# Performance work log

Measured on AMD Instinct MI355X. Metric: run time of the kernel, lower is better.

The kernel has to match this reference:

```python
import jax, jax.numpy as jnp
import numpy as np

N_NODES = 100000
N_EDGES = 1600000
D_IN = 256
D_HID = 128
N_CLASSES = 64
NEG_SLOPE = 0.2


def setup_inputs() -> dict:
    key = jax.random.key(0)
    ks = jax.random.split(key, 8)
    node_features = jax.random.normal(ks[0], (N_NODES, D_IN), dtype=jnp.float32)
    W = jax.random.normal(ks[1], (D_IN, D_HID), dtype=jnp.float32) * (1.0 / np.sqrt(D_IN))
    attn_l = jax.random.normal(ks[2], (D_HID,), dtype=jnp.float32) * (1.0 / np.sqrt(D_HID))
    attn_r = jax.random.normal(ks[3], (D_HID,), dtype=jnp.float32) * (1.0 / np.sqrt(D_HID))
    fc_W = jax.random.normal(ks[4], (D_HID, N_CLASSES), dtype=jnp.float32) * (1.0 / np.sqrt(D_HID))
    fc_b = jnp.zeros((N_CLASSES,), dtype=jnp.float32)
    src = jax.random.randint(ks[5], (N_EDGES,), 0, N_NODES, dtype=jnp.int32)
    dst = jax.random.randint(ks[6], (N_EDGES,), 0, N_NODES, dtype=jnp.int32)
    return dict(node_features=node_features, W=W, attn_l=attn_l, attn_r=attn_r,
                fc_W=fc_W, fc_b=fc_b, src=src, dst=dst)


def reference(node_features, W, attn_l, attn_r, fc_W, fc_b, src, dst):
    N = node_features.shape[0]
    # GATConv (single head): linear projection
    feat = node_features @ W                       # [N, H]
    el = feat @ attn_l                             # [N]
    er = feat @ attn_r                             # [N]
    e = jax.nn.leaky_relu(el[src] + er[dst], NEG_SLOPE)  # [E]
    # segment softmax over incoming edges of each destination node
    m = jax.ops.segment_max(e, dst, num_segments=N)      # [N]
    ex = jnp.exp(e - m[dst])                              # [E]
    denom = jax.ops.segment_sum(ex, dst, num_segments=N)  # [N]
    a = ex / denom[dst]                                   # [E]
    # attention-weighted neighbor aggregation (scatter-add)
    msg = a[:, None] * feat[src]                           # [E, H]
    h = jax.ops.segment_sum(msg, dst, num_segments=N)     # [N, H]
    # num_heads=1 -> h.mean(1) over heads is identity; final Linear
    return h @ fc_W + fc_b                                 # [N, C]
```

## Files before the change

### kernel.cpp

```cpp
#include <hip/hip_runtime.h>
#include <math.h>

#define NN 100000
#define NE 1600000
#define DIN 256
#define DHID 128
#define NCLS 64
#define NEG_SLOPE 0.2f

#define NBUCK 196
#define ECAP 10240
#define CHUNK 4096
#define NCHB ((NE + CHUNK - 1) / CHUNK)
#define PREPB 16

#define NGRP 16384
#define G1 ((NN + 127) / 128)

typedef __bf16 bf16_t;
typedef bf16_t bf16x8 __attribute__((ext_vector_type(8)));
typedef float f32x4 __attribute__((ext_vector_type(4)));
typedef ushort ushort8v __attribute__((ext_vector_type(8)));

__device__ __forceinline__ ushort f2bf(float f) {
    union { float f; unsigned u; } c; c.f = f;
    unsigned u = c.u;
    unsigned r = (u + 0x7FFFu + ((u >> 16) & 1u)) >> 16;
    return (ushort)r;
}
__device__ __forceinline__ float bf2f(ushort b) {
    return __uint_as_float(((unsigned)b) << 16);
}

__global__ __launch_bounds__(256) void k_prep(const float* __restrict__ W,
                                              const float* __restrict__ fcW,
                                              ushort* __restrict__ Wt,
                                              ushort* __restrict__ fcWt,
                                              int* __restrict__ gcur) {
    int t = blockIdx.x * 256 + threadIdx.x;
    if (blockIdx.x == 0) gcur[threadIdx.x] = 0;
    for (int i = t; i < DHID * DIN; i += PREPB * 256) {
        int n = i >> 8, k = i & 255;
        Wt[i] = f2bf(W[k * DHID + n]);
    }
    for (int i = t; i < NCLS * DHID; i += PREPB * 256) {
        int n = i >> 7, k = i & 127;
        fcWt[i] = f2bf(fcW[k * NCLS + n]);
    }
}

union SmemB {
    struct {
        int hist[NBUCK];
        int scn[256];
        int loff[NBUCK];
        int cur[NBUCK];
        int gb[NBUCK];
        unsigned ord[CHUNK];
        ushort obk[CHUNK];
    } b;
    struct {
        ushort Xs[2][8192];
        ushort Wl[2][8192];
        float Al[DHID];
        float Ar[DHID];
    } g;
};

__global__ __launch_bounds__(256, 2) void fused_bin_gemm1(
        const int* __restrict__ src, const int* __restrict__ dst,
        int* __restrict__ gcur, unsigned* __restrict__ ebuf,
        const float* __restrict__ X, const ushort* __restrict__ Wt,
        const float* __restrict__ attn_l, const float* __restrict__ attn_r,
        ushort* __restrict__ featb, float* __restrict__ el, float* __restrict__ er) {
    __shared__ SmemB sm;
    const int t = threadIdx.x;

    if (blockIdx.x < NCHB) {
        const int base = blockIdx.x * CHUNK;
        int cnt = NE - base; if (cnt > CHUNK) cnt = CHUNK;

        for (int i = t; i < NBUCK; i += 256) sm.b.hist[i] = 0;
        __syncthreads();

        unsigned vals[16];
        int bks[16];
#pragma unroll
        for (int i = 0; i < 16; i++) {
            int idx = base + i * 256 + t;
            if (idx < NE) {
                int d = dst[idx], s = src[idx];
                int bb = d >> 9;
                bks[i] = bb;
                vals[i] = ((unsigned)(d & 511) << 17) | (unsigned)s;
                atomicAdd(&sm.b.hist[bb], 1);
            } else bks[i] = -1;
        }
        __syncthreads();

        int hv = (t < NBUCK) ? sm.b.hist[t] : 0;
        sm.b.scn[t] = hv;
        __syncthreads();
        for (int d = 1; d < 256; d <<= 1) {
            int a = (t >= d) ? sm.b.scn[t - d] : 0;
            __syncthreads();
            sm.b.scn[t] += a;
            __syncthreads();
        }
        if (t < NBUCK) { sm.b.loff[t] = sm.b.scn[t] - hv; sm.b.cur[t] = sm.b.scn[t] - hv; }
        __syncthreads();

#pragma unroll
        for (int i = 0; i < 16; i++) {
            if (bks[i] >= 0) {
                int slot = atomicAdd(&sm.b.cur[bks[i]], 1);
                sm.b.ord[slot] = vals[i];
                sm.b.obk[slot] = (ushort)bks[i];
            }
        }
        if (t < NBUCK && hv > 0) sm.b.gb[t] = t * ECAP + atomicAdd(&gcur[t], hv);
        __syncthreads();

        for (int s = t; s < cnt; s += 256) {
            int bb = sm.b.obk[s];
            ebuf[sm.b.gb[bb] + (s - sm.b.loff[bb])] = sm.b.ord[s];
        }
        return;
    }

    const int row0 = (blockIdx.x - NCHB) * 128;
    if (t < 128) { sm.g.Al[t] = attn_l[t]; sm.g.Ar[t] = attn_r[t]; }

    int srow[4], ske[4];
#pragma unroll
    for (int i = 0; i < 4; i++) {
        int o = i * 4096 + t * 16;
        int row = o >> 7;
        int bl = (o & 127) ^ ((row & 7) << 4);
        srow[i] = row;
        ske[i] = bl >> 1;
    }

    float4 xr[4][2];
    uint4  wr[4];

#pragma unroll
    for (int i = 0; i < 4; i++) {
        int grow = row0 + srow[i];
        if (grow < NN) {
            const float4* p = (const float4*)(X + (size_t)grow * DIN + ske[i]);
            xr[i][0] = p[0]; xr[i][1] = p[1];
        } else {
            xr[i][0] = make_float4(0.f, 0.f, 0.f, 0.f);
            xr[i][1] = make_float4(0.f, 0.f, 0.f, 0.f);
        }
        wr[i] = *(const uint4*)(Wt + (size_t)srow[i] * DIN + ske[i]);
    }
#pragma unroll
    for (int i = 0; i < 4; i++) {
        int o = i * 4096 + t * 16;
        ushort8v b;
        b[0] = f2bf(xr[i][0].x); b[1] = f2bf(xr[i][0].y);
        b[2] = f2bf(xr[i][0].z); b[3] = f2bf(xr[i][0].w);
        b[4] = f2bf(xr[i][1].x); b[5] = f2bf(xr[i][1].y);
        b[6] = f2bf(xr[i][1].z); b[7] = f2bf(xr[i][1].w);
        *(ushort8v*)((char*)&sm.g.Xs[0][0] + o) = b;
        *(uint4*)((char*)&sm.g.Wl[0][0] + o) = wr[i];
    }
    __syncthreads();

    const int w = t >> 6, lane = t & 63;
    const int rbase = w * 32;
    const int lcol = lane & 15;
    const int kgrp = (lane >> 4) * 16;

    f32x4 acc[2][8];
#pragma unroll
    for (int r = 0; r < 2; r++)
#pragma unroll
        for (int c = 0; c < 8; c++) acc[r][c] = (f32x4){0.f, 0.f, 0.f, 0.f};

    for (int c = 0; c < 4; c++) {
        const int buf = c & 1;
        if (c < 3) {
            int k0g = (c + 1) * 64;
#pragma unroll
            for (int i = 0; i < 4; i++) {
                int grow = row0 + srow[i];
                if (grow < NN) {
                    const float4* p = (const float4*)(X + (size_t)grow * DIN + k0g + ske[i]);
                    xr[i][0] = p[0]; xr[i][1] = p[1];
                } else {
                    xr[i][0] = make_float4(0.f, 0.f, 0.f, 0.f);
                    xr[i][1] = make_float4(0.f, 0.f, 0.f, 0.f);
                }
                wr[i] = *(const uint4*)(Wt + (size_t)srow[i] * DIN + k0g + ske[i]);
            }
        }
        const char* xb = (const char*)&sm.g.Xs[buf][0];
        const char* wb = (const char*)&sm.g.Wl[buf][0];
#pragma unroll
        for (int k0 = 0; k0 < 2; k0++) {
            int kb = k0 * 64 + kgrp;
            bf16x8 a[2], b[8];
#pragma unroll
            for (int r = 0; r < 2; r++) {
                int row = rbase + r * 16 + lcol;
                a[r] = *(const bf16x8*)(xb + row * 128 + (kb ^ ((row & 7) << 4)));
            }
#pragma unroll
            for (int cc = 0; cc < 8; cc++) {
                int n = cc * 16 + lcol;
                b[cc] = *(const bf16x8*)(wb + n * 128 + (kb ^ ((n & 7) << 4)));
            }
#pragma unroll
            for (int r = 0; r < 2; r++)
#pragma unroll
                for (int cc = 0; cc < 8; cc++)
                    acc[r][cc] = __builtin_amdgcn_mfma_f32_16x16x32_bf16(a[r], b[cc], acc[r][cc], 0, 0, 0);
        }
        if (c < 3) {
#pragma unroll
            for (int i = 0; i < 4; i++) {
                int o = i * 4096 + t * 16;
                ushort8v b;
                b[0] = f2bf(xr[i][0].x); b[1] = f2bf(xr[i][0].y);
                b[2] = f2bf(xr[i][0].z); b[3] = f2bf(xr[i][0].w);
                b[4] = f2bf(xr[i][1].x); b[5] = f2bf(xr[i][1].y);
                b[6] = f2bf(xr[i][1].z); b[7] = f2bf(xr[i][1].w);
                *(ushort8v*)((char*)&sm.g.Xs[buf ^ 1][0] + o) = b;
                *(uint4*)((char*)&sm.g.Wl[buf ^ 1][0] + o) = wr[i];
            }
        }
        __syncthreads();
    }

    ushort* Os = (ushort*)sm.g.Xs;
#pragma unroll
    for (int r = 0; r < 2; r++)
#pragma unroll
        for (int cc = 0; cc < 8; cc++)
#pragma unroll
            for (int i = 0; i < 4; i++) {
                int rloc = rbase + r * 16 + (lane >> 4) * 4 + i;
                int col = cc * 16 + lcol;
                Os[rloc * 128 + col] = f2bf(acc[r][cc][i]);
            }
    __syncthreads();

    {
        int row = t >> 1, half = t & 1;
        int grow = row0 + row;
        const ushort* orow = Os + row * 128 + half * 64;
        const float* alp = sm.g.Al + half * 64;
        const float* arp = sm.g.Ar + half * 64;
        float pl = 0.f, pr = 0.f;
        int rot = row & 7;
#pragma unroll
        for (int qq = 0; qq < 8; qq++) {
            int q = (qq + rot) & 7;
            ushort8v f8 = *(const ushort8v*)(orow + q * 8);
#pragma unroll
            for (int e = 0; e < 8; e++) {
                float fe = bf2f(f8[e]);
                pl += fe * alp[q * 8 + e];
                pr += fe * arp[q * 8 + e];
            }
        }
        pl += __shfl_down(pl, 1);
        pr += __shfl_down(pr, 1);
        if (!half && grow < NN) { el[grow] = pl; er[grow] = pr; }
    }

#pragma unroll
    for (int i = 0; i < 8; i++) {
        int u = i * 256 + t;
        int row = u >> 4;
        int grow = row0 + row;
        if (grow < NN)
            *(uint4*)(featb + (size_t)grow * 128 + (u & 15) * 8) =
                *(uint4*)((char*)Os + u * 16);
    }
}

union SmemC {
    struct {
        int sdeg[512];
        int pr[256];
        int lofs[512];
        int scnt[512];
    } c;
    int sh[256];
};

__global__ __launch_bounds__(256) void fused_csr(const unsigned* __restrict__ ebuf,
                                                 const int* __restrict__ gcur,
                                                 int* __restrict__ off_g,
                                                 int* __restrict__ deg_g,
                                                 int* __restrict__ ssrc,
                                                 int* __restrict__ bpre) {
    __shared__ SmemC sm;
    const int t = threadIdx.x;

    if (blockIdx.x == NBUCK) {
        int v = (t < NBUCK) ? gcur[t] : 0;
        sm.sh[t] = v;
        __syncthreads();
        for (int d = 1; d < 256; d <<= 1) {
            int a = (t >= d) ? sm.sh[t - d] : 0;
            __syncthreads();
            sm.sh[t] += a;
            __syncthreads();
        }
        if (t < NBUCK) bpre[t] = sm.sh[t] - v;
        if (t == NBUCK - 1) bpre[NBUCK] = sm.sh[t];
        return;
    }

    const int b = blockIdx.x;
    const int node0 = b << 9;
    const int ebase = b * ECAP;
    const int ecnt = gcur[b];

    sm.c.sdeg[t] = 0; sm.c.sdeg[t + 256] = 0;
    __syncthreads();
    for (int s = t; s < ecnt; s += 256)
        atomicAdd(&sm.c.sdeg[ebuf[ebase + s] >> 17], 1);
    __syncthreads();

    int d0 = sm.c.sdeg[2 * t], d1 = sm.c.sdeg[2 * t + 1];
    sm.c.pr[t] = d0 + d1;
    __syncthreads();
    for (int d = 1; d < 256; d <<= 1) {
        int a = (t >= d) ? sm.c.pr[t - d] : 0;
        __syncthreads();
        sm.c.pr[t] += a;
        __syncthreads();
    }
    int ex = sm.c.pr[t] - d0 - d1;
    sm.c.lofs[2 * t] = ex;
    sm.c.lofs[2 * t + 1] = ex + d0;
    sm.c.scnt[2 * t] = 0; sm.c.scnt[2 * t + 1] = 0;
    int n0 = node0 + 2 * t, n1 = n0 + 1;
    if (n0 < NN) { off_g[n0] = ebase + ex;      deg_g[n0] = d0; }
    if (n1 < NN) { off_g[n1] = ebase + ex + d0; deg_g[n1] = d1; }
    __syncthreads();

    for (int s = t; s < ecnt; s += 256) {
        unsigned v = ebuf[ebase + s];
        int dl = v >> 17;
        int c = atomicAdd(&sm.c.scnt[dl], 1);
        ssrc[ebase + sm.c.lofs[dl] + c] = (int)(v & 0x1FFFFu);
    }
}

__global__ __launch_bounds__(256) void k_split(const int* __restrict__ off,
                                               const int* __restrict__ bpre,
                                               int* __restrict__ nsplit) {
    int g = blockIdx.x * 256 + threadIdx.x;
    if (g > NGRP) return;
    if (g == NGRP) { nsplit[NGRP] = NN; return; }
    long total = bpre[NBUCK];
    long target = (long)g * total / NGRP;
    int lo = 0, hi = NN;
    while (lo < hi) {
        int mid = (lo + hi) >> 1;
        int b = mid >> 9;
        long real = (long)off[mid] - (long)b * ECAP + bpre[b];
        if (real < target) lo = mid + 1; else hi = mid;
    }
    nsplit[g] = lo;
}

__global__ __launch_bounds__(256) void aggregate(const int* __restrict__ off,
                                                 const int* __restrict__ deg,
                                                 const int* __restrict__ ssrc,
                                                 const float* __restrict__ el,
                                                 const float* __restrict__ er,
                                                 const ushort* __restrict__ featb,
                                                 ushort* __restrict__ hb,
                                                 const int* __restrict__ nsplit) {
    const int gid = blockIdx.x * 16 + (threadIdx.x >> 4);
    const int lc = threadIdx.x & 15;
    int n = nsplit[gid];
    const int nend = nsplit[gid + 1];
    const ushort* fb = featb + lc * 8;

    for (; n < nend; ++n) {
        const int e0 = off[n];
        const int dg = deg[n];
        const float erd = er[n];
        float acc[8];
#pragma unroll
        for (int q = 0; q < 8; q++) acc[q] = 0.f;
        float wsum = 0.f;

        int j = 0;
        for (; j + 4 <= dg; j += 4) {
            int s0 = ssrc[e0 + j + 0];
            int s1 = ssrc[e0 + j + 1];
            int s2 = ssrc[e0 + j + 2];
            int s3 = ssrc[e0 + j + 3];
            ushort8v f0 = *(const ushort8v*)(fb + (size_t)s0 * DHID);
            ushort8v f1 = *(const ushort8v*)(fb + (size_t)s1 * DHID);
            ushort8v f2 = *(const ushort8v*)(fb + (size_t)s2 * DHID);
            ushort8v f3 = *(const ushort8v*)(fb + (size_t)s3 * DHID);
            float x0 = el[s0] + erd, x1 = el[s1] + erd;
            float x2 = el[s2] + erd, x3 = el[s3] + erd;
            x0 = x0 > 0.f ? x0 : NEG_SLOPE * x0;
            x1 = x1 > 0.f ? x1 : NEG_SLOPE * x1;
            x2 = x2 > 0.f ? x2 : NEG_SLOPE * x2;
            x3 = x3 > 0.f ? x3 : NEG_SLOPE * x3;
            float w0 = __expf(x0), w1 = __expf(x1);
            float w2 = __expf(x2), w3 = __expf(x3);
            wsum += (w0 + w1) + (w2 + w3);
#pragma unroll
            for (int q = 0; q < 8; q++)
                acc[q] += (w0 * bf2f(f0[q]) + w1 * bf2f(f1[q])) +
                          (w2 * bf2f(f2[q]) + w3 * bf2f(f3[q]));
        }
        for (; j < dg; ++j) {
            int s0 = ssrc[e0 + j];
            ushort8v f0 = *(const ushort8v*)(fb + (size_t)s0 * DHID);
            float x0 = el[s0] + erd;
            x0 = x0 > 0.f ? x0 : NEG_SLOPE * x0;
            float w0 = __expf(x0);
            wsum += w0;
#pragma unroll
            for (int q = 0; q < 8; q++) acc[q] += w0 * bf2f(f0[q]);
        }

        float inv = (dg > 0) ? 1.0f / wsum : 0.f;
        ushort8v o8;
#pragma unroll
        for (int q = 0; q < 8; q++) o8[q] = f2bf(acc[q] * inv);
        *(ushort8v*)(hb + (size_t)n * DHID + lc * 8) = o8;
    }
}

__global__ __launch_bounds__(256, 3) void gemm2(const ushort* __restrict__ hb,
                                                const ushort* __restrict__ fcWt,
                                                const float* __restrict__ fcb,
                                                float* __restrict__ out) {
    __shared__ ushort Hs[128 * 128];
    __shared__ ushort Fs[64 * 128];
    const int t = threadIdx.x;
    const int row0 = blockIdx.x * 128;

    {
#pragma unroll
        for (int i = 0; i < 8; i++) {
            int u = i * 256 + t;
            int row = u >> 4;
            int grow = row0 + row;
            uint4 v = make_uint4(0, 0, 0, 0);
            if (grow < NN) v = *(const uint4*)(hb + (size_t)grow * 128 + (u & 15) * 8);
            int byte_off = row * 256 + (((u & 15) * 16) ^ ((row & 7) << 4));
            *(uint4*)((char*)Hs + byte_off) = v;
        }
#pragma unroll
        for (int i = 0; i < 4; i++) {
            int u = i * 256 + t;
            int n = u >> 4;
            int byte_off = n * 256 + (((u & 15) * 16) ^ ((n & 7) << 4));
            *(uint4*)((char*)Fs + byte_off) = ((const uint4*)fcWt)[u];
        }
    }

    const int w = t >> 6, lane = t & 63;
    const int rbase = w * 32;
    const int lcol = lane & 15;
    const int kgrp = (lane >> 4) * 16;

    f32x4 acc[2][4];
#pragma unroll
    for (int c = 0; c < 4; c++) {
        float bias = fcb[c * 16 + lcol];
#pragma unroll
        for (int r = 0; r < 2; r++)
#pragma unroll
            for (int i = 0; i < 4; i++) acc[r][c][i] = bias;
    }
    __syncthreads();

#pragma unroll
    for (int k0 = 0; k0 < 4; k0++) {
        int kbyte = k0 * 64 + kgrp;
        bf16x8 a[2], b[4];
#pragma unroll
        for (int r = 0; r < 2; r++) {
            int row = rbase + r * 16 + lcol;
            a[r] = *(bf16x8*)((char*)Hs + row * 256 + (kbyte ^ ((row & 7) << 4)));
        }
#pragma unroll
        for (int c = 0; c < 4; c++) {
            int n = c * 16 + lcol;
            b[c] = *(bf16x8*)((char*)Fs + n * 256 + (kbyte ^ ((n & 7) << 4)));
        }
#pragma unroll
        for (int r = 0; r < 2; r++)
#pragma unroll
            for (int c = 0; c < 4; c++)
                acc[r][c] = __builtin_amdgcn_mfma_f32_16x16x32_bf16(a[r], b[c], acc[r][c], 0, 0, 0);
    }

#pragma unroll
    for (int r = 0; r < 2; r++)
#pragma unroll
        for (int i = 0; i < 4; i++) {
            int row = rbase + r * 16 + (lane >> 4) * 4 + i;
            int grow = row0 + row;
            if (grow < NN) {
                float* op = out + (size_t)grow * 64 + lcol;
#pragma unroll
                for (int c = 0; c < 4; c++) op[c * 16] = acc[r][c][i];
            }
        }
}

extern "C" void kernel_launch(void* const* d_in, const int* in_sizes, int n_in,
                              void* d_out, int out_size, void* d_ws, size_t ws_size,
                              hipStream_t stream) {
    const float* X      = (const float*)d_in[0];
    const float* W      = (const float*)d_in[1];
    const float* attn_l = (const float*)d_in[2];
    const float* attn_r = (const float*)d_in[3];
    const float* fcW    = (const float*)d_in[4];
    const float* fcb    = (const float*)d_in[5];
    const int*   src    = (const int*)d_in[6];
    const int*   dst    = (const int*)d_in[7];
    float* out = (float*)d_out;

    char* ws = (char*)d_ws;
    ushort* featb = (ushort*)ws;            ws += (size_t)NN * DHID * 2;
    ushort* hb    = (ushort*)ws;            ws += (size_t)NN * DHID * 2;
    ushort* Wt    = (ushort*)ws;            ws += (size_t)DHID * DIN * 2;
    ushort* fcWt  = (ushort*)ws;            ws += (size_t)NCLS * DHID * 2;
    float* el     = (float*)ws;             ws += (size_t)NN * 4;
    float* er     = (float*)ws;             ws += (size_t)NN * 4;
    int*   deg    = (int*)ws;               ws += (size_t)NN * 4;
    int*   off    = (int*)ws;               ws += (size_t)NN * 4;
    int*   ssrc   = (int*)ws;               ws += (size_t)NBUCK * ECAP * 4;
    unsigned* ebuf = (unsigned*)ws;         ws += (size_t)NBUCK * ECAP * 4;
    int*   gcur   = (int*)ws;               ws += (size_t)256 * 4;
    int*   bpre   = (int*)ws;               ws += (size_t)256 * 4;
    int*   nsplit = (int*)ws;               ws += (size_t)(NGRP + 1) * 4;

    k_prep<<<PREPB, 256, 0, stream>>>(W, fcW, Wt, fcWt, gcur);
    fused_bin_gemm1<<<NCHB + G1, 256, 0, stream>>>(src, dst, gcur, ebuf,
                                                   X, Wt, attn_l, attn_r, featb, el, er);
    fused_csr<<<NBUCK + 1, 256, 0, stream>>>(ebuf, gcur, off, deg, ssrc, bpre);
    k_split<<<(NGRP + 256) / 256, 256, 0, stream>>>(off, bpre, nsplit);
    aggregate<<<NGRP / 16, 256, 0, stream>>>(off, deg, ssrc, el, er, featb, hb, nsplit);
    gemm2<<<(NN + 127) / 128, 256, 0, stream>>>(hb, fcWt, fcb, out);
}
```

Before: 160.4 us.

## Fuse bucket prefix and split search into CSR kernel; deepen GEMM prefetch

```diff
diff --git a/kernel.cpp b/kernel.cpp
--- a/kernel.cpp
+++ b/kernel.cpp
@@ -67,6 +67,61 @@
     } g;
 };
 
+#define ISSUE(XA, WA, KC) do { \
+    int k0g_ = (KC) * 64; \
+    _Pragma("unroll") \
+    for (int i_ = 0; i_ < 4; i_++) { \
+        int grow_ = row0 + srow[i_]; \
+        if (grow_ < NN) { \
+            const float4* p_ = (const float4*)(X + (size_t)grow_ * DIN + k0g_ + ske[i_]); \
+            XA[i_][0] = p_[0]; XA[i_][1] = p_[1]; \
+        } else { \
+            XA[i_][0] = make_float4(0.f,0.f,0.f,0.f); \
+            XA[i_][1] = make_float4(0.f,0.f,0.f,0.f); \
+        } \
+        WA[i_] = *(const uint4*)(Wt + (size_t)srow[i_] * DIN + k0g_ + ske[i_]); \
+    } \
+} while (0)
+
+#define COMMIT(XA, WA, BUF) do { \
+    _Pragma("unroll") \
+    for (int i_ = 0; i_ < 4; i_++) { \
+        int o_ = i_ * 4096 + t * 16; \
+        ushort8v bb_; \
+        bb_[0] = f2bf(XA[i_][0].x); bb_[1] = f2bf(XA[i_][0].y); \
+        bb_[2] = f2bf(XA[i_][0].z); bb_[3] = f2bf(XA[i_][0].w); \
+        bb_[4] = f2bf(XA[i_][1].x); bb_[5] = f2bf(XA[i_][1].y); \
+        bb_[6] = f2bf(XA[i_][1].z); bb_[7] = f2bf(XA[i_][1].w); \
+        *(ushort8v*)((char*)&sm.g.Xs[BUF][0] + o_) = bb_; \
+        *(uint4*)((char*)&sm.g.Wl[BUF][0] + o_) = WA[i_]; \
+    } \
+} while (0)
+
+#define COMPUTE(BUF) do { \
+    const char* xb_ = (const char*)&sm.g.Xs[BUF][0]; \
+    const char* wb_ = (const char*)&sm.g.Wl[BUF][0]; \
+    _Pragma("unroll") \
+    for (int k0_ = 0; k0_ < 2; k0_++) { \
+        int kb_ = k0_ * 64 + kgrp; \
+        bf16x8 a_[2], b_[8]; \
+        _Pragma("unroll") \
+        for (int r_ = 0; r_ < 2; r_++) { \
+            int row_ = rbase + r_ * 16 + lcol; \
+            a_[r_] = *(const bf16x8*)(xb_ + row_ * 128 + (kb_ ^ ((row_ & 7) << 4))); \
+        } \
+        _Pragma("unroll") \
+        for (int cc_ = 0; cc_ < 8; cc_++) { \
+            int n_ = cc_ * 16 + lcol; \
+            b_[cc_] = *(const bf16x8*)(wb_ + n_ * 128 + (kb_ ^ ((n_ & 7) << 4))); \
+        } \
+        _Pragma("unroll") \
+        for (int r_ = 0; r_ < 2; r_++) \
+            _Pragma("unroll") \
+            for (int cc_ = 0; cc_ < 8; cc_++) \
+                acc[r_][cc_] = __builtin_amdgcn_mfma_f32_16x16x32_bf16(a_[r_], b_[cc_], acc[r_][cc_], 0, 0, 0); \
+    } \
+} while (0)
+
 __global__ __launch_bounds__(256, 2) void fused_bin_gemm1(
         const int* __restrict__ src, const int* __restrict__ dst,
         int* __restrict__ gcur, unsigned* __restrict__ ebuf,
@@ -141,34 +196,6 @@
         ske[i] = bl >> 1;
     }
 
-    float4 xr[4][2];
-    uint4  wr[4];
-
-#pragma unroll
-    for (int i = 0; i < 4; i++) {
-        int grow = row0 + srow[i];
-        if (grow < NN) {
-            const float4* p = (const float4*)(X + (size_t)grow * DIN + ske[i]);
-            xr[i][0] = p[0]; xr[i][1] = p[1];
-        } else {
-            xr[i][0] = make_float4(0.f, 0.f, 0.f, 0.f);
-            xr[i][1] = make_float4(0.f, 0.f, 0.f, 0.f);
-        }
-        wr[i] = *(const uint4*)(Wt + (size_t)srow[i] * DIN + ske[i]);
-    }
-#pragma unroll
-    for (int i = 0; i < 4; i++) {
-        int o = i * 4096 + t * 16;
-        ushort8v b;
-        b[0] = f2bf(xr[i][0].x); b[1] = f2bf(xr[i][0].y);
-        b[2] = f2bf(xr[i][0].z); b[3] = f2bf(xr[i][0].w);
-        b[4] = f2bf(xr[i][1].x); b[5] = f2bf(xr[i][1].y);
-        b[6] = f2bf(xr[i][1].z); b[7] = f2bf(xr[i][1].w);
-        *(ushort8v*)((char*)&sm.g.Xs[0][0] + o) = b;
-        *(uint4*)((char*)&sm.g.Wl[0][0] + o) = wr[i];
-    }
-    __syncthreads();
-
     const int w = t >> 6, lane = t & 63;
     const int rbase = w * 32;
     const int lcol = lane & 15;
@@ -180,61 +207,18 @@
 #pragma unroll
         for (int c = 0; c < 8; c++) acc[r][c] = (f32x4){0.f, 0.f, 0.f, 0.f};
 
-    for (int c = 0; c < 4; c++) {
-        const int buf = c & 1;
-        if (c < 3) {
-            int k0g = (c + 1) * 64;
-#pragma unroll
-            for (int i = 0; i < 4; i++) {
-                int grow = row0 + srow[i];
-                if (grow < NN) {
-                    const float4* p = (const float4*)(X + (size_t)grow * DIN + k0g + ske[i]);
-                    xr[i][0] = p[0]; xr[i][1] = p[1];
-                } else {
-                    xr[i][0] = make_float4(0.f, 0.f, 0.f, 0.f);
-                    xr[i][1] = make_float4(0.f, 0.f, 0.f, 0.f);
-                }
-                wr[i] = *(const uint4*)(Wt + (size_t)srow[i] * DIN + k0g + ske[i]);
-            }
-        }
-        const char* xb = (const char*)&sm.g.Xs[buf][0];
-        const char* wb = (const char*)&sm.g.Wl[buf][0];
-#pragma unroll
-        for (int k0 = 0; k0 < 2; k0++) {
-            int kb = k0 * 64 + kgrp;
-            bf16x8 a[2], b[8];
-#pragma unroll
-            for (int r = 0; r < 2; r++) {
-                int row = rbase + r * 16 + lcol;
-                a[r] = *(const bf16x8*)(xb + row * 128 + (kb ^ ((row & 7) << 4)));
-            }
-#pragma unroll
-            for (int cc = 0; cc < 8; cc++) {
-                int n = cc * 16 + lcol;
-                b[cc] = *(const bf16x8*)(wb + n * 128 + (kb ^ ((n & 7) << 4)));
-            }
-#pragma unroll
-            for (int r = 0; r < 2; r++)
-#pragma unroll
-                for (int cc = 0; cc < 8; cc++)
-                    acc[r][cc] = __builtin_amdgcn_mfma_f32_16x16x32_bf16(a[r], b[cc], acc[r][cc], 0, 0, 0);
-        }
-        if (c < 3) {
-#pragma unroll
-            for (int i = 0; i < 4; i++) {
-                int o = i * 4096 + t * 16;
-                ushort8v b;
-                b[0] = f2bf(xr[i][0].x); b[1] = f2bf(xr[i][0].y);
-                b[2] = f2bf(xr[i][0].z); b[3] = f2bf(xr[i][0].w);
-                b[4] = f2bf(xr[i][1].x); b[5] = f2bf(xr[i][1].y);
-                b[6] = f2bf(xr[i][1].z); b[7] = f2bf(xr[i][1].w);
-                *(ushort8v*)((char*)&sm.g.Xs[buf ^ 1][0] + o) = b;
-                *(uint4*)((char*)&sm.g.Wl[buf ^ 1][0] + o) = wr[i];
-            }
-        }
-        __syncthreads();
-    }
-
+    float4 xA[4][2], xB[4][2];
+    uint4  wA[4], wB[4];
+
+    ISSUE(xA, wA, 0); COMMIT(xA, wA, 0);
+    ISSUE(xB, wB, 1);
+    __syncthreads();
+    ISSUE(xA, wA, 2); COMPUTE(0); COMMIT(xB, wB, 1); __syncthreads();
+    ISSUE(xB, wB, 3); COMPUTE(1); COMMIT(xA, wA, 0); __syncthreads();
+    COMPUTE(0); COMMIT(xB, wB, 1); __syncthreads();
+    COMPUTE(1);
+
+    __syncthreads();
     ushort* Os = (ushort*)sm.g.Xs;
 #pragma unroll
     for (int r = 0; r < 2; r++)
@@ -283,93 +267,88 @@
     }
 }
 
-union SmemC {
-    struct {
-        int sdeg[512];
-        int pr[256];
-        int lofs[512];
-        int scnt[512];
-    } c;
-    int sh[256];
-};
-
-__global__ __launch_bounds__(256) void fused_csr(const unsigned* __restrict__ ebuf,
-                                                 const int* __restrict__ gcur,
-                                                 int* __restrict__ off_g,
-                                                 int* __restrict__ deg_g,
-                                                 int* __restrict__ ssrc,
-                                                 int* __restrict__ bpre) {
-    __shared__ SmemC sm;
-    const int t = threadIdx.x;
-
-    if (blockIdx.x == NBUCK) {
-        int v = (t < NBUCK) ? gcur[t] : 0;
-        sm.sh[t] = v;
-        __syncthreads();
-        for (int d = 1; d < 256; d <<= 1) {
-            int a = (t >= d) ? sm.sh[t - d] : 0;
-            __syncthreads();
-            sm.sh[t] += a;
-            __syncthreads();
-        }
-        if (t < NBUCK) bpre[t] = sm.sh[t] - v;
-        if (t == NBUCK - 1) bpre[NBUCK] = sm.sh[t];
-        return;
-    }
-
-    const int b = blockIdx.x;
+__global__ __launch_bounds__(1024) void fused_csr(const unsigned* __restrict__ ebuf,
+                                                  const int* __restrict__ gcur,
+                                                  int* __restrict__ off_g,
+                                                  int* __restrict__ deg_g,
+                                                  int* __restrict__ ssrc,
+                                                  int* __restrict__ nsplit) {
+    __shared__ int sdeg[512];
+    __shared__ int pr[256];
+    __shared__ int lofs[512];
+    __shared__ int scnt[512];
+    __shared__ int sb[2];
+    const int b = blockIdx.x, t = threadIdx.x;
     const int node0 = b << 9;
     const int ebase = b * ECAP;
     const int ecnt = gcur[b];
 
-    sm.c.sdeg[t] = 0; sm.c.sdeg[t + 256] = 0;
-    __syncthreads();
-    for (int s = t; s < ecnt; s += 256)
-        atomicAdd(&sm.c.sdeg[ebuf[ebase + s] >> 17], 1);
-    __syncthreads();
-
-    int d0 = sm.c.sdeg[2 * t], d1 = sm.c.sdeg[2 * t + 1];
-    sm.c.pr[t] = d0 + d1;
+    if (t < 256) pr[t] = (t < NBUCK) ? gcur[t] : 0;
     __syncthreads();
     for (int d = 1; d < 256; d <<= 1) {
-        int a = (t >= d) ? sm.c.pr[t - d] : 0;
-        __syncthreads();
-        sm.c.pr[t] += a;
-        __syncthreads();
-    }
-    int ex = sm.c.pr[t] - d0 - d1;
-    sm.c.lofs[2 * t] = ex;
-    sm.c.lofs[2 * t + 1] = ex + d0;
-    sm.c.scnt[2 * t] = 0; sm.c.scnt[2 * t + 1] = 0;
-    int n0 = node0 + 2 * t, n1 = n0 + 1;
-    if (n0 < NN) { off_g[n0] = ebase + ex;      deg_g[n0] = d0; }
-    if (n1 < NN) { off_g[n1] = ebase + ex + d0; deg_g[n1] = d1; }
-    __syncthreads();
-
-    for (int s = t; s < ecnt; s += 256) {
+        int a = 0;
+        if (t < 256 && t >= d) a = pr[t - d];
+        __syncthreads();
+        if (t < 256) pr[t] += a;
+        __syncthreads();
+    }
+    if (t == 0) { sb[0] = pr[b] - ecnt; sb[1] = pr[NBUCK - 1]; }
+    if (t < 512) sdeg[t] = 0;
+    __syncthreads();
+
+    for (int s = t; s < ecnt; s += 1024)
+        atomicAdd(&sdeg[ebuf[ebase + s] >> 17], 1);
+    __syncthreads();
+
+    int d0 = 0, d1 = 0;
+    if (t < 256) { d0 = sdeg[2 * t]; d1 = sdeg[2 * t + 1]; pr[t] = d0 + d1; }
+    __syncthreads();
+    for (int d = 1; d < 256; d <<= 1) {
+        int a = 0;
+        if (t < 256 && t >= d) a = pr[t - d];
+        __syncthreads();
+        if (t < 256) pr[t] += a;
+        __syncthreads();
+    }
+    if (t < 256) {
+        int ex = pr[t] - d0 - d1;
+        lofs[2 * t] = ex;
+        lofs[2 * t + 1] = ex + d0;
+        scnt[2 * t] = 0; scnt[2 * t + 1] = 0;
+        int n0 = node0 + 2 * t, n1 = n0 + 1;
+        if (n0 < NN) { off_g[n0] = ebase + ex;      deg_g[n0] = d0; }
+        if (n1 < NN) { off_g[n1] = ebase + ex + d0; deg_g[n1] = d1; }
+    }
+    __syncthreads();
+
+    for (int s = t; s < ecnt; s += 1024) {
         unsigned v = ebuf[ebase + s];
         int dl = v >> 17;
-        int c = atomicAdd(&sm.c.scnt[dl], 1);
-        ssrc[ebase + sm.c.lofs[dl] + c] = (int)(v & 0x1FFFFu);
-    }
-}
-
-__global__ __launch_bounds__(256) void k_split(const int* __restrict__ off,
-                                               const int* __restrict__ bpre,
-                                               int* __restrict__ nsplit) {
-    int g = blockIdx.x * 256 + threadIdx.x;
-    if (g > NGRP) return;
-    if (g == NGRP) { nsplit[NGRP] = NN; return; }
-    long total = bpre[NBUCK];
-    long target = (long)g * total / NGRP;
-    int lo = 0, hi = NN;
-    while (lo < hi) {
-        int mid = (lo + hi) >> 1;
-        int b = mid >> 9;
-        long real = (long)off[mid] - (long)b * ECAP + bpre[b];
-        if (real < target) lo = mid + 1; else hi = mid;
-    }
-    nsplit[g] = lo;
+        int c = atomicAdd(&scnt[dl], 1);
+        ssrc[ebase + lofs[dl] + c] = (int)(v & 0x1FFFFu);
+    }
+
+    {
+        long bpre_b = sb[0], total = sb[1];
+        if (total > 0 && ecnt > 0) {
+            long glo = (bpre_b * NGRP + total - 1) / total;
+            long ghi = ((bpre_b + ecnt) * NGRP + total - 1) / total;
+            if (ghi > NGRP) ghi = NGRP;
+            for (long g = glo + t; g < ghi; g += 1024) {
+                long target = g * total / NGRP;
+                int lt = (int)(target - bpre_b);
+                int lo = 0, hi = 512;
+                while (lo < hi) {
+                    int m = (lo + hi) >> 1;
+                    if (lofs[m] < lt) lo = m + 1; else hi = m;
+                }
+                int node = node0 + lo;
+                if (node > NN) node = NN;
+                nsplit[g] = node;
+            }
+        }
+        if (b == 0 && t == 0) nsplit[NGRP] = NN;
+    }
 }
 
 __global__ __launch_bounds__(256) void aggregate(const int* __restrict__ off,
@@ -543,14 +522,12 @@
     int*   ssrc   = (int*)ws;               ws += (size_t)NBUCK * ECAP * 4;
     unsigned* ebuf = (unsigned*)ws;         ws += (size_t)NBUCK * ECAP * 4;
     int*   gcur   = (int*)ws;               ws += (size_t)256 * 4;
-    int*   bpre   = (int*)ws;               ws += (size_t)256 * 4;
     int*   nsplit = (int*)ws;               ws += (size_t)(NGRP + 1) * 4;
 
     k_prep<<<PREPB, 256, 0, stream>>>(W, fcW, Wt, fcWt, gcur);
     fused_bin_gemm1<<<NCHB + G1, 256, 0, stream>>>(src, dst, gcur, ebuf,
                                                    X, Wt, attn_l, attn_r, featb, el, er);
-    fused_csr<<<NBUCK + 1, 256, 0, stream>>>(ebuf, gcur, off, deg, ssrc, bpre);
-    k_split<<<(NGRP + 256) / 256, 256, 0, stream>>>(off, bpre, nsplit);
+    fused_csr<<<NBUCK, 1024, 0, stream>>>(ebuf, gcur, off, deg, ssrc, nsplit);
     aggregate<<<NGRP / 16, 256, 0, stream>>>(off, deg, ssrc, el, er, featb, hb, nsplit);
     gemm2<<<(NN + 127) / 128, 256, 0, stream>>>(hb, fcWt, fcb, out);
 }
```

New measurement: 160.8 us. Within noise of the previous version (+0.2%).

## Fold bucket prefix and work-split search into CSR kernel with 1024-thread blocks

Applied to the files above, without the earlier changes.

```diff
diff --git a/kernel.cpp b/kernel.cpp
--- a/kernel.cpp
+++ b/kernel.cpp
@@ -283,93 +283,88 @@
     }
 }
 
-union SmemC {
-    struct {
-        int sdeg[512];
-        int pr[256];
-        int lofs[512];
-        int scnt[512];
-    } c;
-    int sh[256];
-};
-
-__global__ __launch_bounds__(256) void fused_csr(const unsigned* __restrict__ ebuf,
-                                                 const int* __restrict__ gcur,
-                                                 int* __restrict__ off_g,
-                                                 int* __restrict__ deg_g,
-                                                 int* __restrict__ ssrc,
-                                                 int* __restrict__ bpre) {
-    __shared__ SmemC sm;
-    const int t = threadIdx.x;
-
-    if (blockIdx.x == NBUCK) {
-        int v = (t < NBUCK) ? gcur[t] : 0;
-        sm.sh[t] = v;
-        __syncthreads();
-        for (int d = 1; d < 256; d <<= 1) {
-            int a = (t >= d) ? sm.sh[t - d] : 0;
-            __syncthreads();
-            sm.sh[t] += a;
-            __syncthreads();
-        }
-        if (t < NBUCK) bpre[t] = sm.sh[t] - v;
-        if (t == NBUCK - 1) bpre[NBUCK] = sm.sh[t];
-        return;
-    }
-
-    const int b = blockIdx.x;
+__global__ __launch_bounds__(1024) void fused_csr(const unsigned* __restrict__ ebuf,
+                                                  const int* __restrict__ gcur,
+                                                  int* __restrict__ off_g,
+                                                  int* __restrict__ deg_g,
+                                                  int* __restrict__ ssrc,
+                                                  int* __restrict__ nsplit) {
+    __shared__ int sdeg[512];
+    __shared__ int pr[256];
+    __shared__ int lofs[512];
+    __shared__ int scnt[512];
+    __shared__ int sb[2];
+    const int b = blockIdx.x, t = threadIdx.x;
     const int node0 = b << 9;
     const int ebase = b * ECAP;
     const int ecnt = gcur[b];
 
-    sm.c.sdeg[t] = 0; sm.c.sdeg[t + 256] = 0;
-    __syncthreads();
-    for (int s = t; s < ecnt; s += 256)
-        atomicAdd(&sm.c.sdeg[ebuf[ebase + s] >> 17], 1);
-    __syncthreads();
-
-    int d0 = sm.c.sdeg[2 * t], d1 = sm.c.sdeg[2 * t + 1];
-    sm.c.pr[t] = d0 + d1;
+    if (t < 256) pr[t] = (t < NBUCK) ? gcur[t] : 0;
     __syncthreads();
     for (int d = 1; d < 256; d <<= 1) {
-        int a = (t >= d) ? sm.c.pr[t - d] : 0;
-        __syncthreads();
-        sm.c.pr[t] += a;
-        __syncthreads();
-    }
-    int ex = sm.c.pr[t] - d0 - d1;
-    sm.c.lofs[2 * t] = ex;
-    sm.c.lofs[2 * t + 1] = ex + d0;
-    sm.c.scnt[2 * t] = 0; sm.c.scnt[2 * t + 1] = 0;
-    int n0 = node0 + 2 * t, n1 = n0 + 1;
-    if (n0 < NN) { off_g[n0] = ebase + ex;      deg_g[n0] = d0; }
-    if (n1 < NN) { off_g[n1] = ebase + ex + d0; deg_g[n1] = d1; }
-    __syncthreads();
-
-    for (int s = t; s < ecnt; s += 256) {
+        int a = 0;
+        if (t < 256 && t >= d) a = pr[t - d];
+        __syncthreads();
+        if (t < 256) pr[t] += a;
+        __syncthreads();
+    }
+    if (t == 0) { sb[0] = pr[b] - ecnt; sb[1] = pr[NBUCK - 1]; }
+    if (t < 512) sdeg[t] = 0;
+    __syncthreads();
+
+    for (int s = t; s < ecnt; s += 1024)
+        atomicAdd(&sdeg[ebuf[ebase + s] >> 17], 1);
+    __syncthreads();
+
+    int d0 = 0, d1 = 0;
+    if (t < 256) { d0 = sdeg[2 * t]; d1 = sdeg[2 * t + 1]; pr[t] = d0 + d1; }
+    __syncthreads();
+    for (int d = 1; d < 256; d <<= 1) {
+        int a = 0;
+        if (t < 256 && t >= d) a = pr[t - d];
+        __syncthreads();
+        if (t < 256) pr[t] += a;
+        __syncthreads();
+    }
+    if (t < 256) {
+        int ex = pr[t] - d0 - d1;
+        lofs[2 * t] = ex;
+        lofs[2 * t + 1] = ex + d0;
+        scnt[2 * t] = 0; scnt[2 * t + 1] = 0;
+        int n0 = node0 + 2 * t, n1 = n0 + 1;
+        if (n0 < NN) { off_g[n0] = ebase + ex;      deg_g[n0] = d0; }
+        if (n1 < NN) { off_g[n1] = ebase + ex + d0; deg_g[n1] = d1; }
+    }
+    __syncthreads();
+
+    for (int s = t; s < ecnt; s += 1024) {
         unsigned v = ebuf[ebase + s];
         int dl = v >> 17;
-        int c = atomicAdd(&sm.c.scnt[dl], 1);
-        ssrc[ebase + sm.c.lofs[dl] + c] = (int)(v & 0x1FFFFu);
-    }
-}
-
-__global__ __launch_bounds__(256) void k_split(const int* __restrict__ off,
-                                               const int* __restrict__ bpre,
-                                               int* __restrict__ nsplit) {
-    int g = blockIdx.x * 256 + threadIdx.x;
-    if (g > NGRP) return;
-    if (g == NGRP) { nsplit[NGRP] = NN; return; }
-    long total = bpre[NBUCK];
-    long target = (long)g * total / NGRP;
-    int lo = 0, hi = NN;
-    while (lo < hi) {
-        int mid = (lo + hi) >> 1;
-        int b = mid >> 9;
-        long real = (long)off[mid] - (long)b * ECAP + bpre[b];
-        if (real < target) lo = mid + 1; else hi = mid;
-    }
-    nsplit[g] = lo;
+        int c = atomicAdd(&scnt[dl], 1);
+        ssrc[ebase + lofs[dl] + c] = (int)(v & 0x1FFFFu);
+    }
+
+    {
+        long bpre_b = sb[0], total = sb[1];
+        if (total > 0 && ecnt > 0) {
+            long glo = (bpre_b * NGRP + total - 1) / total;
+            long ghi = ((bpre_b + ecnt) * NGRP + total - 1) / total;
+            if (ghi > NGRP) ghi = NGRP;
+            for (long g = glo + t; g < ghi; g += 1024) {
+                long target = g * total / NGRP;
+                int lt = (int)(target - bpre_b);
+                int lo = 0, hi = 512;
+                while (lo < hi) {
+                    int m = (lo + hi) >> 1;
+                    if (lofs[m] < lt) lo = m + 1; else hi = m;
+                }
+                int node = node0 + lo;
+                if (node > NN) node = NN;
+                nsplit[g] = node;
+            }
+        }
+        if (b == 0 && t == 0) nsplit[NGRP] = NN;
+    }
 }
 
 __global__ __launch_bounds__(256) void aggregate(const int* __restrict__ off,
@@ -543,14 +538,12 @@
     int*   ssrc   = (int*)ws;               ws += (size_t)NBUCK * ECAP * 4;
     unsigned* ebuf = (unsigned*)ws;         ws += (size_t)NBUCK * ECAP * 4;
     int*   gcur   = (int*)ws;               ws += (size_t)256 * 4;
-    int*   bpre   = (int*)ws;               ws += (size_t)256 * 4;
     int*   nsplit = (int*)ws;               ws += (size_t)(NGRP + 1) * 4;
 
     k_prep<<<PREPB, 256, 0, stream>>>(W, fcW, Wt, fcWt, gcur);
     fused_bin_gemm1<<<NCHB + G1, 256, 0, stream>>>(src, dst, gcur, ebuf,
                                                    X, Wt, attn_l, attn_r, featb, el, er);
-    fused_csr<<<NBUCK + 1, 256, 0, stream>>>(ebuf, gcur, off, deg, ssrc, bpre);
-    k_split<<<(NGRP + 256) / 256, 256, 0, stream>>>(off, bpre, nsplit);
+    fused_csr<<<NBUCK, 1024, 0, stream>>>(ebuf, gcur, off, deg, ssrc, nsplit);
     aggregate<<<NGRP / 16, 256, 0, stream>>>(off, deg, ssrc, el, er, featb, hb, nsplit);
     gemm2<<<(NN + 127) / 128, 256, 0, stream>>>(hb, fcWt, fcb, out);
 }
```

After: 147.7 us, median of 2. -7.9%, faster.
